# Kernel optimization log

Measured on AMD Instinct MI355X. Metric: run time of the kernel, lower is better.

The kernel has to match this reference:

```python
import jax, jax.numpy as jnp
import numpy as np

D_MODEL = 768
N_HEADS = 12
D_KEYS = 64
D_LLM = 4096
D_INNER = N_HEADS * D_KEYS  # 768


def setup_inputs() -> dict:
    key = jax.random.key(0)
    ks = jax.random.split(key, 12)
    inp = {
        "target_embedding": jax.random.normal(ks[0], (8, 1024, D_MODEL), dtype=jnp.float32),
        "source_embedding": jax.random.normal(ks[1], (1000, D_LLM), dtype=jnp.float32),
        "value_embedding": jax.random.normal(ks[2], (1000, D_LLM), dtype=jnp.float32),
        # Linear params stored as [in, out] (y = x @ W + b)
        "Wq": jax.random.normal(ks[3], (D_MODEL, D_INNER), dtype=jnp.float32) * 0.02,
        "bq": jnp.zeros((D_INNER,), dtype=jnp.float32),
        "Wk": jax.random.normal(ks[4], (D_LLM, D_INNER), dtype=jnp.float32) * 0.02,
        "bk": jnp.zeros((D_INNER,), dtype=jnp.float32),
        "Wv": jax.random.normal(ks[5], (D_LLM, D_INNER), dtype=jnp.float32) * 0.02,
        "bv": jnp.zeros((D_INNER,), dtype=jnp.float32),
        "Wo": jax.random.normal(ks[6], (D_INNER, D_LLM), dtype=jnp.float32) * 0.02,
        "bo": jnp.zeros((D_LLM,), dtype=jnp.float32),
    }
    return inp


def reference(target_embedding, source_embedding, value_embedding,
              Wq, bq, Wk, bk, Wv, bv, Wo, bo):
    B, L, _ = target_embedding.shape
    S, _ = source_embedding.shape
    H, E = N_HEADS, D_KEYS
    # projections
    q = (target_embedding @ Wq + bq).reshape(B, L, H, E)  # [B,L,H,E]
    k = (source_embedding @ Wk + bk).reshape(S, H, E)     # [S,H,E] broadcast over batch
    v = (value_embedding @ Wv + bv).reshape(S, H, E)      # [S,H,E]
    scale = 1.0 / np.sqrt(E).astype(np.float32)
    scores = jnp.einsum('blhe,she->bhls', q, k) * scale   # [B,H,L,S]
    A = jax.nn.softmax(scores, axis=-1)                   # dropout is identity at eval
    out = jnp.einsum('bhls,she->blhe', A, v).reshape(B, L, H * E)
    return out @ Wo + bo                                  # [B,L,d_llm]
```

## Files before the change

### kernel.cpp

```cpp
#include <hip/hip_runtime.h>
#include <cstdint>
#include <type_traits>


typedef unsigned short u16;
typedef __attribute__((ext_vector_type(8))) short bf16x8;
typedef __attribute__((ext_vector_type(4))) float f32x4;
typedef __attribute__((ext_vector_type(16))) float f32x16;
typedef __attribute__((ext_vector_type(4))) float fvec4;
typedef __attribute__((ext_vector_type(4))) unsigned short u16x4;
typedef __attribute__((ext_vector_type(4))) unsigned int u32x4;
typedef __attribute__((ext_vector_type(2))) unsigned int u32x2;

using gld_src_t = const __attribute__((address_space(1))) void*;
using gld_dst_t = __attribute__((address_space(3))) void*;

static __device__ __forceinline__ u16 bf16_rne(float f) {
  uint32_t u = __builtin_bit_cast(uint32_t, f);
  u += 0x7fffu + ((u >> 16) & 1u);
  return (u16)(u >> 16);
}

static __device__ __forceinline__ float exp2_fast(float x) {
  float r; asm("v_exp_f32 %0, %1" : "=v"(r) : "v"(x)); return r;
}

static __device__ __forceinline__ uint32_t pk_bf16(float a, float b) {
  return (uint32_t)bf16_rne(a) | ((uint32_t)bf16_rne(b) << 16);
}

__global__ void convert_pad_bf16(const float* __restrict__ in, u16* __restrict__ out,
                                 int validR, int C, long n4) {
  long stride = (long)gridDim.x * blockDim.x;
  for (long i = (long)blockIdx.x * blockDim.x + threadIdx.x; i < n4; i += stride) {
    long e = i << 2;
    int r = (int)(e / C);
    u16x4 o;
    if (r < validR) {
      fvec4 v = *(const fvec4*)(in + e);
      o[0] = bf16_rne(v[0]); o[1] = bf16_rne(v[1]);
      o[2] = bf16_rne(v[2]); o[3] = bf16_rne(v[3]);
    } else {
      o[0] = 0; o[1] = 0; o[2] = 0; o[3] = 0;
    }
    *(u16x4*)(out + e) = o;
  }
}

template <bool F32IN>
__global__ void transpose_to_bf16(const void* __restrict__ inv, u16* __restrict__ out,
                                  int R, int C) {
  __shared__ u16 tile[32][33];
  int bc = blockIdx.x * 32, br = blockIdx.y * 32;
  int tx = threadIdx.x & 31, ty = threadIdx.x >> 5;
#pragma unroll
  for (int i = 0; i < 4; ++i) {
    int r = br + ty + i * 8, c = bc + tx;
    u16 bits = 0;
    if (r < R && c < C) {
      if constexpr (F32IN) bits = bf16_rne(((const float*)inv)[(size_t)r * C + c]);
      else                 bits = ((const u16*)inv)[(size_t)r * C + c];
    }
    tile[ty + i * 8][tx] = bits;
  }
  __syncthreads();
#pragma unroll
  for (int i = 0; i < 4; ++i) {
    int orow = bc + ty + i * 8, oc = br + tx;
    if (orow < C && oc < R) out[(size_t)orow * R + oc] = tile[tx][ty + i * 8];
  }
}

template <typename CT>
__global__ __launch_bounds__(256, 2) void gemm_bt_128p(
    const u16* __restrict__ A, const u16* __restrict__ B,
    const float* __restrict__ bias, CT* __restrict__ C,
    int N, int K, float escale) {
  __shared__ u16 As[2][128 * 64];
  __shared__ u16 Bs[2][128 * 64];

  const int tid = threadIdx.x, lane = tid & 63, w = tid >> 6;
  const int lr = lane & 15, lg = lane >> 4;
  const int wr = (w >> 1) * 64, wc = (w & 1) * 64;

  const int nbx = N >> 7;
  const int bid = blockIdx.y * gridDim.x + blockIdx.x;
  const int cpx = (gridDim.x * gridDim.y) >> 3;
  const int swz = (bid & 7) * cpx + (bid >> 3);
  const int bm = (swz / nbx) * 128, bn = (swz % nbx) * 128;

  f32x4 acc[4][4] = {};

  auto STAGE = [&](int t, int buf) {
#pragma unroll
    for (int it = 0; it < 4; ++it) {
      const int s = it * 256 + tid;
      const int r = s >> 3;
      const int cg = (s & 7) ^ (r & 7);
      const int ldsb = (it * 256 + w * 64) * 16;
      __builtin_amdgcn_global_load_lds(
          (gld_src_t)(const void*)(A + (size_t)(bm + r) * K + t * 64 + cg * 8),
          (gld_dst_t)((char*)&As[buf][0] + ldsb), 16, 0, 0);
      __builtin_amdgcn_global_load_lds(
          (gld_src_t)(const void*)(B + (size_t)(bn + r) * K + t * 64 + cg * 8),
          (gld_dst_t)((char*)&Bs[buf][0] + ldsb), 16, 0, 0);
    }
  };

  auto LDF = [&](const u16* base, int R, int CB) {
    return *(const bf16x8*)((const char*)base + (size_t)R * 128 + (CB ^ ((R & 7) << 4)));
  };

  STAGE(0, 0);

  const int nk = K >> 6;
  for (int t = 0; t < nk; ++t) {
    const int cur = t & 1;
    if (t + 1 < nk) {
      STAGE(t + 1, cur ^ 1);
      asm volatile("s_waitcnt vmcnt(8)" ::: "memory");
    } else {
      asm volatile("s_waitcnt vmcnt(0)" ::: "memory");
    }
    __builtin_amdgcn_s_barrier();
    __builtin_amdgcn_sched_barrier(0);

    const u16* as = &As[cur][0];
    const u16* bs = &Bs[cur][0];

    bf16x8 af[4][2], bfr[4][2];
#pragma unroll
    for (int m = 0; m < 4; ++m)
#pragma unroll
      for (int kk = 0; kk < 2; ++kk)
        af[m][kk] = LDF(as, wr + m * 16 + lr, kk * 64 + lg * 16);
#pragma unroll
    for (int n = 0; n < 4; ++n)
#pragma unroll
      for (int kk = 0; kk < 2; ++kk)
        bfr[n][kk] = LDF(bs, wc + n * 16 + lr, kk * 64 + lg * 16);

    __builtin_amdgcn_s_setprio(1);
#pragma unroll
    for (int kk = 0; kk < 2; ++kk)
#pragma unroll
      for (int m = 0; m < 4; ++m)
#pragma unroll
        for (int n = 0; n < 4; ++n)
          acc[m][n] = __builtin_amdgcn_mfma_f32_16x16x32_bf16(
              af[m][kk], bfr[n][kk], acc[m][n], 0, 0, 0);
    __builtin_amdgcn_s_setprio(0);

    __builtin_amdgcn_sched_barrier(0);
    __builtin_amdgcn_s_barrier();
  }

#pragma unroll
  for (int n = 0; n < 4; ++n) {
    const int col = bn + wc + n * 16 + lr;
    const float bv = bias[col];
#pragma unroll
    for (int m = 0; m < 4; ++m) {
      const int row0 = bm + wr + m * 16 + lg * 4;
#pragma unroll
      for (int r = 0; r < 4; ++r) {
        float v = (acc[m][n][r] + bv) * escale;
        if constexpr (std::is_same<CT, u16>::value)
          C[(size_t)(row0 + r) * N + col] = bf16_rne(v);
        else
          C[(size_t)(row0 + r) * N + col] = v;
      }
    }
  }
}

__global__ __launch_bounds__(256) void gemm_kv_splitk(
    const u16* __restrict__ Sb, const u16* __restrict__ Vbi,
    const u16* __restrict__ WkT, const u16* __restrict__ WvT,
    float* __restrict__ part) {
  const int z = blockIdx.z;
  const u16* A = (z >> 2) ? Vbi : Sb;
  const u16* B = (z >> 2) ? WvT : WkT;
  float* C = part + (size_t)z * (1024 * 768);
  const int kofs = (z & 3) * 1024;

  __shared__ u16 As[128 * 32];
  __shared__ u16 Bs[128 * 32];
  const int tid = threadIdx.x, w = tid >> 6, lane = tid & 63;
  const int lr = lane & 15, lg = lane >> 4;
  const int bm = blockIdx.y * 128, bn = blockIdx.x * 128;
  const int wr = (w >> 1) * 64, wc = (w & 1) * 64;
  f32x4 acc[4][4] = {};

  for (int kt = 0; kt < 32; ++kt) {
#pragma unroll
    for (int j = 0; j < 2; ++j) {
      int cb = j * 256 + w * 64;
      int c = cb + lane;
      const u16* gA = A + (size_t)(bm + (c >> 2)) * 4096 + kofs + kt * 32 + (c & 3) * 8;
      __builtin_amdgcn_global_load_lds((gld_src_t)(const void*)gA,
                                       (gld_dst_t)(As + (size_t)cb * 8), 16, 0, 0);
      const u16* gB = B + (size_t)(bn + (c >> 2)) * 4096 + kofs + kt * 32 + (c & 3) * 8;
      __builtin_amdgcn_global_load_lds((gld_src_t)(const void*)gB,
                                       (gld_dst_t)(Bs + (size_t)cb * 8), 16, 0, 0);
    }
    __syncthreads();
    bf16x8 af[4], bfr[4];
#pragma unroll
    for (int m = 0; m < 4; ++m)
      af[m] = *(const bf16x8*)(As + (wr + m * 16 + lr) * 32 + lg * 8);
#pragma unroll
    for (int n = 0; n < 4; ++n)
      bfr[n] = *(const bf16x8*)(Bs + (wc + n * 16 + lr) * 32 + lg * 8);
#pragma unroll
    for (int m = 0; m < 4; ++m)
#pragma unroll
      for (int n = 0; n < 4; ++n)
        acc[m][n] = __builtin_amdgcn_mfma_f32_16x16x32_bf16(af[m], bfr[n], acc[m][n], 0, 0, 0);
    __syncthreads();
  }
#pragma unroll
  for (int n = 0; n < 4; ++n) {
    int col = bn + wc + n * 16 + lr;
#pragma unroll
    for (int m = 0; m < 4; ++m) {
      int row0 = bm + wr + m * 16 + lg * 4;
#pragma unroll
      for (int r = 0; r < 4; ++r)
        C[(size_t)(row0 + r) * 768 + col] = acc[m][n][r];
    }
  }
}

__global__ __launch_bounds__(256) void kv_reduce(const float* __restrict__ part,
                                                 const float* __restrict__ bk,
                                                 const float* __restrict__ bv,
                                                 u16* __restrict__ Kp, u16* __restrict__ Vp) {
  const int mat = blockIdx.y;
  const long e = ((long)blockIdx.x * 256 + threadIdx.x) * 4;
  const float* p0 = part + (size_t)mat * 4 * 786432 + e;
  fvec4 s = *(const fvec4*)p0;
  s += *(const fvec4*)(p0 + 786432);
  s += *(const fvec4*)(p0 + 2 * 786432);
  s += *(const fvec4*)(p0 + 3 * 786432);
  const float* bias = mat ? bv : bk;
  int col = (int)(e % 768);
  fvec4 bb = *(const fvec4*)(bias + col);
  s += bb;
  u16x4 o;
  o[0] = bf16_rne(s[0]); o[1] = bf16_rne(s[1]); o[2] = bf16_rne(s[2]); o[3] = bf16_rne(s[3]);
  u16* dst = mat ? Vp : Kp;
  *(u16x4*)(dst + e) = o;
}

__global__ __launch_bounds__(256, 3) void attn_flash(
    const u16* __restrict__ Q,
    const u16* __restrict__ Kb,
    const u16* __restrict__ VT,
    u16* __restrict__ O) {
  constexpr int DM = 768, SPAD = 1024;
  __shared__ u16 Ks[2][64 * 64];
  __shared__ u16 VTs[2][64 * 64];

  const int tid = threadIdx.x, w = tid >> 6, lane = tid & 63;
  const int q5 = lane & 31, hi = lane >> 5, l7 = lane & 7;
  const int h = blockIdx.y;
  const int qrow = blockIdx.x * 128 + w * 32 + q5;

  bf16x8 qf[4];
#pragma unroll
  for (int dstep = 0; dstep < 4; ++dstep)
    qf[dstep] = *(const bf16x8*)(Q + (size_t)qrow * DM + h * 64 + dstep * 16 + hi * 8);

  auto STAGE = [&](int ch, int buf) {
#pragma unroll
    for (int it = 0; it < 2; ++it) {
      int slot = it * 256 + w * 64 + lane;
      int row = slot >> 3;
      int cg = (slot & 7) ^ (row & 7);
      __builtin_amdgcn_global_load_lds(
          (gld_src_t)(const void*)(Kb + (size_t)(ch * 64 + row) * DM + h * 64 + cg * 8),
          (gld_dst_t)(&Ks[buf][(size_t)(it * 256 + w * 64) * 8]), 16, 0, 0);
      __builtin_amdgcn_global_load_lds(
          (gld_src_t)(const void*)(VT + (size_t)(h * 64 + row) * SPAD + ch * 64 + cg * 8),
          (gld_dst_t)(&VTs[buf][(size_t)(it * 256 + w * 64) * 8]), 16, 0, 0);
    }
  };

  STAGE(0, 0);

  float m_run = -3.0e38f, l_part = 0.0f;
  f32x16 oa0 = {}, oa1 = {};

  for (int ch = 0; ch < 16; ++ch) {
    const int cur = ch & 1;
    if (ch < 15) {
      STAGE(ch + 1, cur ^ 1);
      asm volatile("s_waitcnt vmcnt(4)" ::: "memory");
    } else {
      asm volatile("s_waitcnt vmcnt(0)" ::: "memory");
    }
    __builtin_amdgcn_s_barrier();
    __builtin_amdgcn_sched_barrier(0);

    const char* kbase = (const char*)&Ks[cur][0];
    const char* vbase = (const char*)&VTs[cur][0];

    f32x16 sc0 = {}, sc1 = {};
#pragma unroll
    for (int dstep = 0; dstep < 4; ++dstep) {
      const int colb = (dstep * 32 + hi * 16);
      bf16x8 kf0 = *(const bf16x8*)(kbase + (size_t)q5 * 128 + (colb ^ (l7 << 4)));
      bf16x8 kf1 = *(const bf16x8*)(kbase + (size_t)(32 + q5) * 128 + (colb ^ (l7 << 4)));
      sc0 = __builtin_amdgcn_mfma_f32_32x32x16_bf16(kf0, qf[dstep], sc0, 0, 0, 0);
      sc1 = __builtin_amdgcn_mfma_f32_32x32x16_bf16(kf1, qf[dstep], sc1, 0, 0, 0);
    }
    if (ch == 15) {
#pragma unroll
      for (int r = 4; r < 16; ++r) sc1[r] = -3.0e38f;
    }

    float mi = sc0[0];
#pragma unroll
    for (int r = 1; r < 16; ++r) mi = fmaxf(mi, sc0[r]);
#pragma unroll
    for (int r = 0; r < 16; ++r) mi = fmaxf(mi, sc1[r]);
    float cm = fmaxf(mi, __shfl_xor(mi, 32, 64));

    if (__any(cm > m_run + 8.0f)) {
      float mn = fmaxf(m_run, cm);
      float fsc = exp2_fast(m_run - mn);
      m_run = mn;
      l_part *= fsc;
#pragma unroll
      for (int r = 0; r < 16; ++r) { oa0[r] *= fsc; oa1[r] *= fsc; }
    }

#pragma unroll
    for (int r = 0; r < 16; ++r) {
      float p0 = exp2_fast(sc0[r] - m_run); l_part += p0; sc0[r] = p0;
      float p1 = exp2_fast(sc1[r] - m_run); l_part += p1; sc1[r] = p1;
    }

#pragma unroll
    for (int st = 0; st < 2; ++st) {
#pragma unroll
      for (int ks = 0; ks < 2; ++ks) {
        float pv0, pv1, pv2, pv3, pv4, pv5, pv6, pv7;
        if (st == 0) {
          if (ks == 0) { pv0=sc0[0];pv1=sc0[1];pv2=sc0[2];pv3=sc0[3];pv4=sc0[4];pv5=sc0[5];pv6=sc0[6];pv7=sc0[7]; }
          else         { pv0=sc0[8];pv1=sc0[9];pv2=sc0[10];pv3=sc0[11];pv4=sc0[12];pv5=sc0[13];pv6=sc0[14];pv7=sc0[15]; }
        } else {
          if (ks == 0) { pv0=sc1[0];pv1=sc1[1];pv2=sc1[2];pv3=sc1[3];pv4=sc1[4];pv5=sc1[5];pv6=sc1[6];pv7=sc1[7]; }
          else         { pv0=sc1[8];pv1=sc1[9];pv2=sc1[10];pv3=sc1[11];pv4=sc1[12];pv5=sc1[13];pv6=sc1[14];pv7=sc1[15]; }
        }
        uint32_t a = pk_bf16(pv0, pv1), b = pk_bf16(pv2, pv3);
        uint32_t c = pk_bf16(pv4, pv5), d = pk_bf16(pv6, pv7);
        uint32_t sa = (uint32_t)__shfl_xor((int)a, 32, 64);
        uint32_t sb = (uint32_t)__shfl_xor((int)b, 32, 64);
        uint32_t sc_ = (uint32_t)__shfl_xor((int)c, 32, 64);
        uint32_t sd = (uint32_t)__shfl_xor((int)d, 32, 64);
        u32x4 jw;
        jw[0] = hi ? sc_ : a;
        jw[1] = hi ? sd  : b;
        jw[2] = hi ? c   : sa;
        jw[3] = hi ? d   : sb;
        bf16x8 pB = __builtin_bit_cast(bf16x8, jw);
        const int colb = (st * 64 + ks * 32 + hi * 16);
#pragma unroll
        for (int dt = 0; dt < 2; ++dt) {
          bf16x8 vtf = *(const bf16x8*)(vbase + (size_t)(dt * 32 + q5) * 128 + (colb ^ (l7 << 4)));
          if (dt == 0) oa0 = __builtin_amdgcn_mfma_f32_32x32x16_bf16(vtf, pB, oa0, 0, 0, 0);
          else         oa1 = __builtin_amdgcn_mfma_f32_32x32x16_bf16(vtf, pB, oa1, 0, 0, 0);
        }
      }
    }
    __builtin_amdgcn_sched_barrier(0);
    __builtin_amdgcn_s_barrier();
  }

  float ool = 1.0f / (l_part + __shfl_xor(l_part, 32, 64));
  u16* obase = O + (size_t)qrow * DM + h * 64;
#pragma unroll
  for (int dt = 0; dt < 2; ++dt) {
#pragma unroll
    for (int g = 0; g < 4; ++g) {
      float v0, v1, v2, v3;
      if (dt == 0) { v0 = oa0[4*g]; v1 = oa0[4*g+1]; v2 = oa0[4*g+2]; v3 = oa0[4*g+3]; }
      else         { v0 = oa1[4*g]; v1 = oa1[4*g+1]; v2 = oa1[4*g+2]; v3 = oa1[4*g+3]; }
      u32x2 st2;
      st2[0] = pk_bf16(v0 * ool, v1 * ool);
      st2[1] = pk_bf16(v2 * ool, v3 * ool);
      *(u32x2*)(obase + dt * 32 + g * 8 + hi * 4) = st2;
    }
  }
}

extern "C" void kernel_launch(void* const* d_in, const int* in_sizes, int n_in,
                              void* d_out, int out_size, void* d_ws, size_t ws_size,
                              hipStream_t stream) {
  (void)in_sizes; (void)n_in; (void)out_size; (void)ws_size;
  const float* target = (const float*)d_in[0];
  const float* source = (const float*)d_in[1];
  const float* value  = (const float*)d_in[2];
  const float* Wq = (const float*)d_in[3];
  const float* bq = (const float*)d_in[4];
  const float* Wk = (const float*)d_in[5];
  const float* bk = (const float*)d_in[6];
  const float* Wv = (const float*)d_in[7];
  const float* bv = (const float*)d_in[8];
  const float* Wo = (const float*)d_in[9];
  const float* bo = (const float*)d_in[10];
  float* out = (float*)d_out;

  char* ws = (char*)d_ws;
  size_t off = 0;
  auto carve = [&](size_t bytes) { void* p = ws + off; off += (bytes + 255) & ~(size_t)255; return p; };
  u16* Xb  = (u16*)carve(8192ull * 768 * 2);
  u16* Sb  = (u16*)carve(1024ull * 4096 * 2);
  u16* Vbi = (u16*)carve(1024ull * 4096 * 2);
  u16* WqT = (u16*)carve(768ull * 768 * 2);
  u16* WkT = (u16*)carve(768ull * 4096 * 2);
  u16* WvT = (u16*)carve(768ull * 4096 * 2);
  u16* WoT = (u16*)carve(4096ull * 768 * 2);
  u16* Qb  = (u16*)carve(8192ull * 768 * 2);
  u16* Kp  = (u16*)carve(1024ull * 768 * 2);
  u16* Vp  = (u16*)carve(1024ull * 768 * 2);
  u16* VTp = (u16*)carve(768ull * 1024 * 2);
  u16* Ob  = (u16*)carve(8192ull * 768 * 2);

  const float SCL = 0.18033688011112042f;

  convert_pad_bf16<<<2048, 256, 0, stream>>>(target, Xb, 8192, 768, (8192ll * 768) / 4);
  convert_pad_bf16<<<2048, 256, 0, stream>>>(source, Sb, 1000, 4096, (1024ll * 4096) / 4);
  convert_pad_bf16<<<2048, 256, 0, stream>>>(value,  Vbi, 1000, 4096, (1024ll * 4096) / 4);
  transpose_to_bf16<true><<<dim3(24, 24),  256, 0, stream>>>(Wq, WqT, 768, 768);
  transpose_to_bf16<true><<<dim3(24, 128), 256, 0, stream>>>(Wk, WkT, 4096, 768);
  transpose_to_bf16<true><<<dim3(24, 128), 256, 0, stream>>>(Wv, WvT, 4096, 768);
  transpose_to_bf16<true><<<dim3(128, 24), 256, 0, stream>>>(Wo, WoT, 768, 4096);

  gemm_kv_splitk<<<dim3(6, 8, 8), 256, 0, stream>>>(Sb, Vbi, WkT, WvT, out);
  kv_reduce<<<dim3(768, 2), 256, 0, stream>>>(out, bk, bv, Kp, Vp);
  transpose_to_bf16<false><<<dim3(24, 32), 256, 0, stream>>>(Vp, VTp, 1024, 768);

  gemm_bt_128p<u16><<<dim3(6, 64), 256, 0, stream>>>(Xb, WqT, bq, Qb, 768, 768, SCL);

  attn_flash<<<dim3(64, 12), 256, 0, stream>>>(Qb, Kp, VTp, Ob);

  gemm_bt_128p<float><<<dim3(32, 64), 256, 0, stream>>>(Ob, WoT, bo, out, 4096, 768, 1.0f);
}
```

Before: 226.6 us.

## Pre-pack B weights into MFMA fragment order and load directly to registers

Adds a packing kernel that reorders the transposed Wq and Wo weights into per-lane MFMA fragment layout, reusing freed workspace buffers. The projection GEMMs then load B fragments straight from global memory into registers with double-buffered register sets, staging only A through LDS. This removes B's LDS traffic and halves the shared-memory footprint. In exchange it adds two pack launches, raises register pressure, and repeats B global reads across warps with no LDS sharing.

```diff
diff --git a/kernel.cpp b/kernel.cpp
--- a/kernel.cpp
+++ b/kernel.cpp
@@ -71,13 +71,21 @@
   }
 }
 
+__global__ void pack_b_frag(const u16* __restrict__ Bt, u16* __restrict__ Bp, int K) {
+  const int idx = blockIdx.x * 256 + threadIdx.x;
+  const int lane = idx & 63, ci = idx >> 6;
+  const int KB = K >> 5;
+  const int nt = ci / KB, kb = ci % KB;
+  const u16* src = Bt + (size_t)(nt * 16 + (lane & 15)) * K + kb * 32 + (lane >> 4) * 8;
+  *(bf16x8*)(Bp + (size_t)idx * 8) = *(const bf16x8*)src;
+}
+
 template <typename CT>
-__global__ __launch_bounds__(256, 2) void gemm_bt_128p(
-    const u16* __restrict__ A, const u16* __restrict__ B,
+__global__ __launch_bounds__(256, 2) void gemm_bt_128g(
+    const u16* __restrict__ A, const u16* __restrict__ Bp,
     const float* __restrict__ bias, CT* __restrict__ C,
     int N, int K, float escale) {
   __shared__ u16 As[2][128 * 64];
-  __shared__ u16 Bs[2][128 * 64];
 
   const int tid = threadIdx.x, lane = tid & 63, w = tid >> 6;
   const int lr = lane & 15, lg = lane >> 4;
@@ -89,9 +97,12 @@
   const int swz = (bid & 7) * cpx + (bid >> 3);
   const int bm = (swz / nbx) * 128, bn = (swz % nbx) * 128;
 
+  const int KB = K >> 5;
+  const int ntg0 = (bn + wc) >> 4;
+
   f32x4 acc[4][4] = {};
 
-  auto STAGE = [&](int t, int buf) {
+  auto STAGE_A = [&](int t, int buf) {
 #pragma unroll
     for (int it = 0; it < 4; ++it) {
       const int s = it * 256 + tid;
@@ -101,45 +112,27 @@
       __builtin_amdgcn_global_load_lds(
           (gld_src_t)(const void*)(A + (size_t)(bm + r) * K + t * 64 + cg * 8),
           (gld_dst_t)((char*)&As[buf][0] + ldsb), 16, 0, 0);
-      __builtin_amdgcn_global_load_lds(
-          (gld_src_t)(const void*)(B + (size_t)(bn + r) * K + t * 64 + cg * 8),
-          (gld_dst_t)((char*)&Bs[buf][0] + ldsb), 16, 0, 0);
     }
   };
-
-  auto LDF = [&](const u16* base, int R, int CB) {
+  auto LOAD_B = [&](int t, bf16x8 (&dst)[4][2]) {
+#pragma unroll
+    for (int n = 0; n < 4; ++n)
+#pragma unroll
+      for (int kk = 0; kk < 2; ++kk)
+        dst[n][kk] = *(const bf16x8*)(
+            Bp + ((size_t)((ntg0 + n) * KB + t * 2 + kk) * 64 + lane) * 8);
+  };
+  auto LDFA = [&](const u16* base, int R, int CB) {
     return *(const bf16x8*)((const char*)base + (size_t)R * 128 + (CB ^ ((R & 7) << 4)));
   };
-
-  STAGE(0, 0);
-
-  const int nk = K >> 6;
-  for (int t = 0; t < nk; ++t) {
-    const int cur = t & 1;
-    if (t + 1 < nk) {
-      STAGE(t + 1, cur ^ 1);
-      asm volatile("s_waitcnt vmcnt(8)" ::: "memory");
-    } else {
-      asm volatile("s_waitcnt vmcnt(0)" ::: "memory");
-    }
-    __builtin_amdgcn_s_barrier();
-    __builtin_amdgcn_sched_barrier(0);
-
-    const u16* as = &As[cur][0];
-    const u16* bs = &Bs[cur][0];
-
-    bf16x8 af[4][2], bfr[4][2];
+  auto COMPUTE = [&](int buf, bf16x8 (&bfr)[4][2]) {
+    const u16* as = &As[buf][0];
+    bf16x8 af[4][2];
 #pragma unroll
     for (int m = 0; m < 4; ++m)
 #pragma unroll
       for (int kk = 0; kk < 2; ++kk)
-        af[m][kk] = LDF(as, wr + m * 16 + lr, kk * 64 + lg * 16);
-#pragma unroll
-    for (int n = 0; n < 4; ++n)
-#pragma unroll
-      for (int kk = 0; kk < 2; ++kk)
-        bfr[n][kk] = LDF(bs, wc + n * 16 + lr, kk * 64 + lg * 16);
-
+        af[m][kk] = LDFA(as, wr + m * 16 + lr, kk * 64 + lg * 16);
     __builtin_amdgcn_s_setprio(1);
 #pragma unroll
     for (int kk = 0; kk < 2; ++kk)
@@ -150,7 +143,37 @@
           acc[m][n] = __builtin_amdgcn_mfma_f32_16x16x32_bf16(
               af[m][kk], bfr[n][kk], acc[m][n], 0, 0, 0);
     __builtin_amdgcn_s_setprio(0);
-
+  };
+
+  bf16x8 b0[4][2], b1[4][2];
+  STAGE_A(0, 0);
+  LOAD_B(0, b0);
+
+  const int nk = K >> 6;
+  for (int t = 0; t < nk; t += 2) {
+    if (t + 1 < nk) {
+      STAGE_A(t + 1, 1);
+      LOAD_B(t + 1, b1);
+      asm volatile("s_waitcnt vmcnt(12)" ::: "memory");
+    } else {
+      asm volatile("s_waitcnt vmcnt(0)" ::: "memory");
+    }
+    __builtin_amdgcn_s_barrier();
+    __builtin_amdgcn_sched_barrier(0);
+    COMPUTE(0, b0);
+    __builtin_amdgcn_sched_barrier(0);
+    __builtin_amdgcn_s_barrier();
+    if (t + 1 >= nk) break;
+    if (t + 2 < nk) {
+      STAGE_A(t + 2, 0);
+      LOAD_B(t + 2, b0);
+      asm volatile("s_waitcnt vmcnt(12)" ::: "memory");
+    } else {
+      asm volatile("s_waitcnt vmcnt(0)" ::: "memory");
+    }
+    __builtin_amdgcn_s_barrier();
+    __builtin_amdgcn_sched_barrier(0);
+    COMPUTE(1, b1);
     __builtin_amdgcn_sched_barrier(0);
     __builtin_amdgcn_s_barrier();
   }
@@ -428,6 +451,8 @@
   u16* Vp  = (u16*)carve(1024ull * 768 * 2);
   u16* VTp = (u16*)carve(768ull * 1024 * 2);
   u16* Ob  = (u16*)carve(8192ull * 768 * 2);
+  u16* Bpo = Sb;
+  u16* Bpq = Vbi;
 
   const float SCL = 0.18033688011112042f;
 
@@ -443,9 +468,12 @@
   kv_reduce<<<dim3(768, 2), 256, 0, stream>>>(out, bk, bv, Kp, Vp);
   transpose_to_bf16<false><<<dim3(24, 32), 256, 0, stream>>>(Vp, VTp, 1024, 768);
 
-  gemm_bt_128p<u16><<<dim3(6, 64), 256, 0, stream>>>(Xb, WqT, bq, Qb, 768, 768, SCL);
+  pack_b_frag<<<1536, 256, 0, stream>>>(WoT, Bpo, 768);
+  pack_b_frag<<<288,  256, 0, stream>>>(WqT, Bpq, 768);
+
+  gemm_bt_128g<u16><<<dim3(6, 64), 256, 0, stream>>>(Xb, Bpq, bq, Qb, 768, 768, SCL);
 
   attn_flash<<<dim3(64, 12), 256, 0, stream>>>(Qb, Kp, VTp, Ob);
 
-  gemm_bt_128p<float><<<dim3(32, 64), 256, 0, stream>>>(Ob, WoT, bo, out, 4096, 768, 1.0f);
-}
+  gemm_bt_128g<float><<<dim3(32, 64), 256, 0, stream>>>(Ob, Bpo, bo, out, 4096, 768, 1.0f);
+}
```

New measurement: 239.8 us. 5.8% more time.

## Use 256x256 tile, 4-stage pipelined GEMM for output projection

Applied to the files above, without the earlier changes.

Replaces the 128x128-tile output projection GEMM with a new 512-thread kernel that computes 256x256 tiles. It uses a 4-deep LDS ring with direct global-to-LDS loads, XOR-swizzled LDS layout, and an XCD-aware block-index swizzle. The larger tile raises operand reuse and cuts global traffic for the biggest GEMM (8192x4096x768). The risks are a smaller grid (512 blocks), which may underfill the GPU, and 128KB of LDS per block limiting occupancy.

```diff
diff --git a/kernel.cpp b/kernel.cpp
--- a/kernel.cpp
+++ b/kernel.cpp
@@ -170,6 +170,103 @@
         else
           C[(size_t)(row0 + r) * N + col] = v;
       }
+    }
+  }
+}
+
+__global__ __launch_bounds__(512, 2) void gemm_bt_256p(
+    const u16* __restrict__ A, const u16* __restrict__ B,
+    const float* __restrict__ bias, float* __restrict__ C,
+    int N, int K) {
+  __shared__ u16 As[4][128 * 64];
+  __shared__ u16 Bs[4][128 * 64];
+
+  const int tid = threadIdx.x, lane = tid & 63, w = tid >> 6;
+  const int lr = lane & 15, lg = lane >> 4;
+  const int wr = w >> 2, wcol = w & 3;
+
+  const int nbx = N >> 8;
+  const int bid = blockIdx.y * gridDim.x + blockIdx.x;
+  const int cpx = (gridDim.x * gridDim.y) >> 3;
+  const int swz = (bid & 7) * cpx + (bid >> 3);
+  const int bm = (swz / nbx) * 256, bn = (swz % nbx) * 256;
+
+  f32x4 acc[8][4] = {};
+
+  auto STAGE_UNIT = [&](int t, int buf, int mat) {
+#pragma unroll
+    for (int it = 0; it < 2; ++it) {
+      const int s = it * 512 + tid;
+      const int rp = s >> 3;
+      const int cl = (s & 7) ^ (rp & 7);
+      const int gr = (cl >> 2) * 128 + rp;
+      const int gc = cl & 3;
+      const int ldsb = (it * 512 + w * 64) * 16;
+      const u16* src = (mat ? B : A) + (size_t)((mat ? bn : bm) + gr) * K + t * 32 + gc * 8;
+      __builtin_amdgcn_global_load_lds((gld_src_t)(const void*)src,
+          (gld_dst_t)((char*)(mat ? &Bs[buf][0] : &As[buf][0]) + ldsb), 16, 0, 0);
+    }
+  };
+
+  auto LDF = [&](const u16* base, int gr, int klg) {
+    const int byte = (gr & 127) * 128 + (((((gr >> 7) * 4 + klg) << 4)) ^ ((gr & 7) << 4));
+    return *(const bf16x8*)((const char*)base + byte);
+  };
+
+  STAGE_UNIT(0, 0, 0); STAGE_UNIT(0, 0, 1);
+  STAGE_UNIT(1, 1, 0); STAGE_UNIT(1, 1, 1);
+  asm volatile("s_waitcnt vmcnt(4)" ::: "memory");
+  __builtin_amdgcn_s_barrier();
+  __builtin_amdgcn_sched_barrier(0);
+
+  const int nk = K >> 5;
+  bf16x8 bfr[4];
+  for (int t = 0; t < nk; ++t) {
+    const int cur = t & 3;
+    const u16* as = &As[cur][0];
+    const u16* bs = &Bs[cur][0];
+#pragma unroll
+    for (int p = 0; p < 2; ++p) {
+      bf16x8 af[4];
+#pragma unroll
+      for (int m = 0; m < 4; ++m)
+        af[m] = LDF(as, wr * 128 + (p * 4 + m) * 16 + lr, lg);
+      if (p == 0) {
+#pragma unroll
+        for (int n = 0; n < 4; ++n)
+          bfr[n] = LDF(bs, wcol * 64 + n * 16 + lr, lg);
+      }
+      if (t + 2 < nk) STAGE_UNIT(t + 2, (t + 2) & 3, p);
+      if (p == 1) {
+        if (t + 2 < nk)      asm volatile("s_waitcnt vmcnt(4)" ::: "memory");
+        else if (t + 1 < nk) asm volatile("s_waitcnt vmcnt(0)" ::: "memory");
+      }
+      __builtin_amdgcn_s_barrier();
+      __builtin_amdgcn_sched_barrier(0);
+      __builtin_amdgcn_s_setprio(1);
+#pragma unroll
+      for (int m = 0; m < 4; ++m)
+#pragma unroll
+        for (int n = 0; n < 4; ++n)
+          acc[p * 4 + m][n] = __builtin_amdgcn_mfma_f32_16x16x32_bf16(
+              af[m], bfr[n], acc[p * 4 + m][n], 0, 0, 0);
+      __builtin_amdgcn_s_setprio(0);
+      __builtin_amdgcn_sched_barrier(0);
+    }
+  }
+
+  float bv[4];
+#pragma unroll
+  for (int nf = 0; nf < 4; ++nf) bv[nf] = bias[bn + wcol * 64 + nf * 16 + lr];
+#pragma unroll
+  for (int mf = 0; mf < 8; ++mf) {
+    const int row0 = bm + wr * 128 + mf * 16 + lg * 4;
+#pragma unroll
+    for (int nf = 0; nf < 4; ++nf) {
+      const int col = bn + wcol * 64 + nf * 16 + lr;
+#pragma unroll
+      for (int r = 0; r < 4; ++r)
+        C[(size_t)(row0 + r) * N + col] = acc[mf][nf][r] + bv[nf];
     }
   }
 }
@@ -447,5 +544,5 @@
 
   attn_flash<<<dim3(64, 12), 256, 0, stream>>>(Qb, Kp, VTp, Ob);
 
-  gemm_bt_128p<float><<<dim3(32, 64), 256, 0, stream>>>(Ob, WoT, bo, out, 4096, 768, 1.0f);
-}
+  gemm_bt_256p<<<dim3(16, 32), 512, 0, stream>>>(Ob, WoT, bo, out, 4096, 768);
+}
```

After: 215.9 us. 4.7% less time.
